# Kernel optimization log

Measured on AMD Instinct MI355X. Metric: run time of the kernel, lower is better.

The kernel has to match this reference:

```python
import jax, jax.numpy as jnp
import numpy as np

EPS = 0.1
MAX_ITER = 100
THRESH = 0.1


def _cost_matrix(x, y):
    # |x_i - y_j|^2 summed over feature dim, via the GEMM identity
    # ||x||^2 + ||y||^2 - 2<x,y>; clamp tiny negatives from fp error.
    x2 = jnp.sum(x * x, axis=-1)[..., :, None]          # (N,P1,1)
    y2 = jnp.sum(y * y, axis=-1)[..., None, :]          # (N,1,P2)
    xy = jnp.einsum('npd,nqd->npq', x, y)               # (N,P1,P2)
    return jnp.maximum(x2 + y2 - 2.0 * xy, 0.0)


def setup_inputs() -> dict:
    key = jax.random.key(0)
    k1, k2 = jax.random.split(key)
    x = jax.random.normal(k1, (8, 1024, 64), dtype=jnp.float32)
    y = jax.random.normal(k2, (8, 1024, 64), dtype=jnp.float32)
    return {"input": x, "target": y}


def reference(input, target):
    x, y = input, target
    C = _cost_matrix(x, y)                               # (N,P1,P2)
    N, P1 = x.shape[0], x.shape[-2]
    P2 = y.shape[-2]
    mu = jnp.full((N, P1), 1.0 / P1, dtype=C.dtype)
    nu = jnp.full((N, P2), 1.0 / P2, dtype=C.dtype)
    log_mu = jnp.log(mu + 1e-8)
    log_nu = jnp.log(nu + 1e-8)

    def M(u, v):
        # (-C + u_i + v_j) / eps
        return (-C + u[..., :, None] + v[..., None, :]) / EPS

    def body(carry, _):
        u, v, done = carry
        u_new = EPS * (log_mu - jax.scipy.special.logsumexp(M(u, v), axis=-1)) + u
        v_new = EPS * (log_nu - jax.scipy.special.logsumexp(M(u_new, v), axis=-2)) + v
        err = jnp.mean(jnp.sum(jnp.abs(u_new - u), axis=-1))
        # apply the update only if not yet converged (matches torch early break,
        # which breaks AFTER the update that achieved err < thresh)
        u = jnp.where(done, u, u_new)
        v = jnp.where(done, v, v_new)
        done = done | (err < THRESH)
        return (u, v, done), None

    u0 = jnp.zeros((N, P1), dtype=C.dtype)
    v0 = jnp.zeros((N, P2), dtype=C.dtype)
    (u, v, _), _ = jax.lax.scan(body, (u0, v0, jnp.array(False)), None, length=MAX_ITER)

    pi = jnp.exp(M(u, v))                                # transport plan (N,P1,P2)
    cost = jnp.sum(pi * C, axis=(-2, -1))                # (N,) with reduction='none'
    return cost
```

## Files before the change

kernel.cpp:

```cpp
#include <hip/hip_runtime.h>
#include <hip/hip_fp16.h>

#define NB 8
#define P 1024
#define D 64
#define EPSF 0.1f
#define INV_EPS 10.0f
#define MAX_IT 100
#define EPS_LOG_MU (-0.693146162f)
#define IB 512
#define TPB_I 512
#define BPB 64

#define HALF_F (NB * P * P / 2)
#define OFF_Z    0
#define OFF_ZT   (HALF_F)
#define OFF_U    (2 * HALF_F)
#define OFF_V    (OFF_U + NB * P)
#define OFF_X2   (OFF_V + NB * P)
#define OFF_Y2   (OFF_X2 + NB * P)
#define OFF_UH   (OFF_Y2 + NB * P)
#define OFF_DU   (OFF_UH + MAX_IT * NB * P)
#define OFF_BAR  (OFF_DU + MAX_IT * IB)
#define OFF_T    (OFF_BAR + 256)
#define OFF_COST (OFF_T + 64)
#define WS_FLOATS (OFF_COST + 64)

__device__ __forceinline__ void publish_f(float* p, float v) {
    __hip_atomic_store(p, v, __ATOMIC_RELAXED, __HIP_MEMORY_SCOPE_SYSTEM);
}

__device__ __forceinline__ void sysld4(float4& w0, float4& w1, float4& w2, float4& w3,
                                       const float* p0, const float* p1,
                                       const float* p2, const float* p3)
{
    asm volatile(
        "global_load_dwordx4 %0, %4, off sc0 sc1\n\t"
        "global_load_dwordx4 %1, %5, off sc0 sc1\n\t"
        "global_load_dwordx4 %2, %6, off sc0 sc1\n\t"
        "global_load_dwordx4 %3, %7, off sc0 sc1\n\t"
        "s_waitcnt vmcnt(0)"
        : "=&v"(w0), "=&v"(w1), "=&v"(w2), "=&v"(w3)
        : "v"(p0), "v"(p1), "v"(p2), "v"(p3)
        : "memory");
}

__global__ __launch_bounds__(256)
void init_k(const float* __restrict__ x, const float* __restrict__ y,
            float* __restrict__ ws)
{
    const int g = blockIdx.x * 256 + threadIdx.x;
    if (g < NB * P) {
        const float4* xr = (const float4*)(x + (size_t)g * D);
        const float4* yr = (const float4*)(y + (size_t)g * D);
        float sx = 0.f, sy = 0.f;
#pragma unroll
        for (int k = 0; k < D / 4; k++) {
            float4 a = xr[k], b = yr[k];
            sx = fmaf(a.x, a.x, fmaf(a.y, a.y, fmaf(a.z, a.z, fmaf(a.w, a.w, sx))));
            sy = fmaf(b.x, b.x, fmaf(b.y, b.y, fmaf(b.z, b.z, fmaf(b.w, b.w, sy))));
        }
        ws[OFF_X2 + g] = sx; ws[OFF_Y2 + g] = sy;
        ws[OFF_U + g] = 0.f; ws[OFF_V + g] = 0.f;
    }
    if (g < 256) ((unsigned*)(ws + OFF_BAR))[g] = 0u;
    if (g < 64)  ws[OFF_COST + g] = 0.f;
}

__global__ __launch_bounds__(256)
void gemm_k(const float* __restrict__ x, const float* __restrict__ y,
            float* __restrict__ ws)
{
    float* x2 = ws + OFF_X2;
    float* y2 = ws + OFF_Y2;
    const int tid   = threadIdx.x;
    const int half_ = blockIdx.x >> 9;
    const int bid   = blockIdx.x & 511;
    const int nB    = bid & 7;
    const int inner = bid >> 3;

    const float* A  = half_ ? y : x;
    const float* B  = half_ ? x : y;
    const float* ra = (half_ ? y2 : x2) + nB * P;
    const float* rb = (half_ ? x2 : y2) + nB * P;
    __half* out = (__half*)(ws + (half_ ? OFF_ZT : OFF_Z)) + (size_t)nB * P * P;

    __shared__ float xs [64 * 68];
    __shared__ float ysT[64 * 64];

    for (int k4 = 0; k4 < 4; k4++) {
        const int t  = inner * 4 + k4;
        const int ti = t >> 4, tj = t & 15;
        const float* abase = A + (size_t)(nB * P + ti * 64) * D;
        const float* bbase = B + (size_t)(nB * P + tj * 64) * D;
#pragma unroll
        for (int k = 0; k < 4; k++) {
            const int f = k * 1024 + tid * 4;
            const int r = f >> 6, c = f & 63;
            float4 a = *(const float4*)(abase + f);
            *(float4*)(xs + r * 68 + c) = a;
            float4 b = *(const float4*)(bbase + f);
            const int pr  = r >> 2;
            const int r3  = r & 3;
            const int t15 = c >> 2;
            ysT[(c + 0) * 64 + (((pr ^ t15) & 15) << 2) + r3] = b.x;
            ysT[(c + 1) * 64 + (((pr ^ t15) & 15) << 2) + r3] = b.y;
            ysT[(c + 2) * 64 + (((pr ^ t15) & 15) << 2) + r3] = b.z;
            ysT[(c + 3) * 64 + (((pr ^ t15) & 15) << 2) + r3] = b.w;
        }
        __syncthreads();
        const int r0 = tid >> 4;
        const int g  = tid & 15;
        const int c0 = g << 2;
#pragma unroll
        for (int rr = 0; rr < 4; rr++) {
            const int row = rr * 16 + r0;
            const float* xrow = xs + row * 68;
            float s0 = 0.f, s1 = 0.f, s2 = 0.f, s3 = 0.f;
#pragma unroll
            for (int d = 0; d < 64; d++) {
                const float xv = xrow[d];
                const float4 yv = *(const float4*)(ysT + d * 64 + ((g ^ ((d >> 2) & 15)) << 2));
                s0 = fmaf(xv, yv.x, s0); s1 = fmaf(xv, yv.y, s1);
                s2 = fmaf(xv, yv.z, s2); s3 = fmaf(xv, yv.w, s3);
            }
            const int gr = ti * 64 + row;
            const int gc = tj * 64 + c0;
            const float xq = ra[gr];
            union { unsigned long long u64; __half h[4]; } p;
            p.h[0] = __float2half_rn(-fmaxf(xq + rb[gc + 0] - 2.f * s0, 0.f) * INV_EPS);
            p.h[1] = __float2half_rn(-fmaxf(xq + rb[gc + 1] - 2.f * s1, 0.f) * INV_EPS);
            p.h[2] = __float2half_rn(-fmaxf(xq + rb[gc + 2] - 2.f * s2, 0.f) * INV_EPS);
            p.h[3] = __float2half_rn(-fmaxf(xq + rb[gc + 3] - 2.f * s3, 0.f) * INV_EPS);
            *(unsigned long long*)(out + (size_t)gr * P + gc) = p.u64;
        }
        __syncthreads();
    }
}

__device__ __forceinline__ void args8(uint4 c, float4 w0, float4 w1, float* zp)
{
    const __half2* h = (const __half2*)&c;
    float2 f;
    f = __half22float2(h[0]); zp[0] = fmaf(w0.x, INV_EPS, f.x); zp[1] = fmaf(w0.y, INV_EPS, f.y);
    f = __half22float2(h[1]); zp[2] = fmaf(w0.z, INV_EPS, f.x); zp[3] = fmaf(w0.w, INV_EPS, f.y);
    f = __half22float2(h[2]); zp[4] = fmaf(w1.x, INV_EPS, f.x); zp[5] = fmaf(w1.y, INV_EPS, f.y);
    f = __half22float2(h[3]); zp[6] = fmaf(w1.z, INV_EPS, f.x); zp[7] = fmaf(w1.w, INV_EPS, f.y);
}

#define MAX4(a,b,c,d) fmaxf(fmaxf(a,b),fmaxf(c,d))

__device__ __forceinline__ void lse2(uint4 c0a, uint4 c0b, uint4 c1a, uint4 c1b,
                                     float4 w0, float4 w1, float4 w2, float4 w3,
                                     float& o0, float& o1)
{
    float z0[16], z1[16];
    args8(c0a, w0, w1, z0); args8(c0b, w2, w3, z0 + 8);
    args8(c1a, w0, w1, z1); args8(c1b, w2, w3, z1 + 8);

    float m0 = fmaxf(MAX4(z0[0], z0[1], z0[2], z0[3]),  MAX4(z0[4], z0[5], z0[6], z0[7]));
    m0 = fmaxf(m0, fmaxf(MAX4(z0[8], z0[9], z0[10], z0[11]), MAX4(z0[12], z0[13], z0[14], z0[15])));
    float m1 = fmaxf(MAX4(z1[0], z1[1], z1[2], z1[3]),  MAX4(z1[4], z1[5], z1[6], z1[7]));
    m1 = fmaxf(m1, fmaxf(MAX4(z1[8], z1[9], z1[10], z1[11]), MAX4(z1[12], z1[13], z1[14], z1[15])));
#pragma unroll
    for (int off = 32; off; off >>= 1) {
        m0 = fmaxf(m0, __shfl_xor(m0, off, 64));
        m1 = fmaxf(m1, __shfl_xor(m1, off, 64));
    }
    float s0, s1;
    {
        float e0[16], e1[16];
#pragma unroll
        for (int q = 0; q < 16; q++) { e0[q] = __expf(z0[q] - m0); e1[q] = __expf(z1[q] - m1); }
#pragma unroll
        for (int q = 0; q < 8; q++)  { e0[q] += e0[q + 8]; e1[q] += e1[q + 8]; }
#pragma unroll
        for (int q = 0; q < 4; q++)  { e0[q] += e0[q + 4]; e1[q] += e1[q + 4]; }
        s0 = (e0[0] + e0[1]) + (e0[2] + e0[3]);
        s1 = (e1[0] + e1[1]) + (e1[2] + e1[3]);
    }
#pragma unroll
    for (int off = 32; off; off >>= 1) {
        s0 += __shfl_xor(s0, off, 64);
        s1 += __shfl_xor(s1, off, 64);
    }
    o0 = EPS_LOG_MU - EPSF * (m0 + __logf(s0));
    o1 = EPS_LOG_MU - EPSF * (m1 + __logf(s1));
}

__device__ __forceinline__ void bbar(unsigned* ctr, unsigned target)
{
    __syncthreads();
    if (threadIdx.x == 0) {
        __builtin_amdgcn_s_waitcnt(0);
        __hip_atomic_fetch_add(ctr, 1u, __ATOMIC_RELAXED, __HIP_MEMORY_SCOPE_AGENT);
        unsigned g = 0;
        while (__hip_atomic_load(ctr, __ATOMIC_RELAXED, __HIP_MEMORY_SCOPE_SYSTEM) < target) {
            __builtin_amdgcn_s_sleep(2);
            if (++g > (1u << 15)) break;
        }
    }
    __syncthreads();
}

__global__ __launch_bounds__(TPB_I, 4)
void iter_k(float* __restrict__ ws)
{
    const __half* z  = (const __half*)(ws + OFF_Z);
    const __half* zT = (const __half*)(ws + OFF_ZT);
    float* uh  = ws + OFF_UH;
    float* v   = ws + OFF_V;
    float* dup = ws + OFF_DU;

    const int tid   = threadIdx.x;
    const int nB    = blockIdx.x & 7;
    const int inner = blockIdx.x >> 3;
    const int wid   = tid >> 6;
    const int lane  = tid & 63;

    __shared__ float duRed[8];

    const int r0 = inner * 16 + wid * 2;
    const size_t zbase = (size_t)nB * P * P;

    const uint4* zr0 = (const uint4*)(z  + zbase + (size_t)(r0    ) * P);
    const uint4* zr1 = (const uint4*)(z  + zbase + (size_t)(r0 + 1) * P);
    const uint4* tr0 = (const uint4*)(zT + zbase + (size_t)(r0    ) * P);
    const uint4* tr1 = (const uint4*)(zT + zbase + (size_t)(r0 + 1) * P);
    const uint4 cz0a = zr0[lane], cz0b = zr0[lane + 64];
    const uint4 cz1a = zr1[lane], cz1b = zr1[lane + 64];
    const uint4 ct0a = tr0[lane], ct0b = tr0[lane + 64];
    const uint4 ct1a = tr1[lane], ct1b = tr1[lane + 64];

    unsigned* ctr = (unsigned*)(ws + OFF_BAR) + nB * 32;
    const int wo = lane * 8;
    float* vb = v + nB * P;

    float uold0 = 0.f, uold1 = 0.f;
    unsigned bstep = 0;

    for (int t = 0; t < MAX_IT; t++) {
        float* ut = uh + (size_t)t * (NB * P) + nB * P;

        float4 w0, w1, w2, w3;
        if (t == 0) {
            w0 = w1 = w2 = w3 = make_float4(0.f, 0.f, 0.f, 0.f);
        } else {
            sysld4(w0, w1, w2, w3, vb + wo, vb + wo + 4, vb + 512 + wo, vb + 512 + wo + 4);
        }
        float un0, un1;
        lse2(cz0a, cz0b, cz1a, cz1b, w0, w1, w2, w3, un0, un1);
        if (lane == 0) {
            publish_f(&ut[r0], un0);
            publish_f(&ut[r0 + 1], un1);
            duRed[wid] = fabsf(un0 - uold0) + fabsf(un1 - uold1);
        }
        uold0 = un0; uold1 = un1;
        __syncthreads();
        if (tid == 0) {
            float d = 0.f;
#pragma unroll
            for (int k = 0; k < 8; k++) d += duRed[k];
            dup[t * IB + blockIdx.x] = d;
        }
        bbar(ctr, BPB * (++bstep));

        float4 q0, q1, q2, q3;
        sysld4(q0, q1, q2, q3, ut + wo, ut + wo + 4, ut + 512 + wo, ut + 512 + wo + 4);
        float vn0, vn1;
        lse2(ct0a, ct0b, ct1a, ct1b, q0, q1, q2, q3, vn0, vn1);
        if (lane == 0) {
            publish_f(&vb[r0], vn0);
            publish_f(&vb[r0 + 1], vn1);
        }
        bbar(ctr, BPB * (++bstep));
    }
}

__global__ __launch_bounds__(1024)
void findT_k(float* __restrict__ ws)
{
    __shared__ float Spart[1024];
    __shared__ float S[MAX_IT];
    __shared__ int Ts;
    const int tid = threadIdx.x;

    {
        const int t = tid >> 3, sub = tid & 7;
        float s = 0.f;
        if (t < MAX_IT) {
            const float* dp = ws + OFF_DU + t * IB + sub * 64;
            for (int i = 0; i < 64; i++) s += dp[i];
        }
        Spart[tid] = s;
    }
    __syncthreads();
    if (tid < MAX_IT) {
        float s = 0.f;
#pragma unroll
        for (int k = 0; k < 8; k++) s += Spart[tid * 8 + k];
        S[tid] = s;
    }
    __syncthreads();
    if (tid == 0) {
        int T = MAX_IT - 1;
        for (int t = 0; t < MAX_IT; t++) if (S[t] < 0.8f) { T = t; break; }
        Ts = T;
        *(int*)(ws + OFF_T) = T;
    }
    __syncthreads();
    const int T = Ts;
    const float* src = ws + OFF_UH + (size_t)T * (NB * P);
    float* u = ws + OFF_U;
    for (int i = tid; i < NB * P; i += 1024) u[i] = src[i];
    if (tid < 64) ws[OFF_COST + tid] = 0.f;
}

__device__ __forceinline__ float lse_row(const __half* mat, const float4* wv,
                                         int row, int lane)
{
    const float4* mr = (const float4*)(mat + (size_t)row * P);
    const float4 ca = mr[lane];
    const float4 cb = mr[lane + 64];
    const uint4* cau = (const uint4*)&ca;
    const uint4* cbu = (const uint4*)&cb;
    const float4 wa0 = wv[2 * lane],       wa1 = wv[2 * lane + 1];
    const float4 wb0 = wv[128 + 2 * lane], wb1 = wv[129 + 2 * lane];
    float zv[16];
    args8(*cau, wa0, wa1, zv);
    args8(*cbu, wb0, wb1, zv + 8);
    float m = fmaxf(MAX4(zv[0], zv[1], zv[2], zv[3]), MAX4(zv[4], zv[5], zv[6], zv[7]));
    m = fmaxf(m, fmaxf(MAX4(zv[8], zv[9], zv[10], zv[11]), MAX4(zv[12], zv[13], zv[14], zv[15])));
#pragma unroll
    for (int off = 32; off; off >>= 1) m = fmaxf(m, __shfl_xor(m, off, 64));
    float s = 0.f;
#pragma unroll
    for (int q = 0; q < 16; q++) s += __expf(zv[q] - m);
#pragma unroll
    for (int off = 32; off; off >>= 1) s += __shfl_xor(s, off, 64);
    return EPS_LOG_MU - EPSF * (m + __logf(s));
}

__global__ __launch_bounds__(256)
void colT_k(float* __restrict__ ws)
{
    const __half* zT = (const __half*)(ws + OFF_ZT);
    float* u = ws + OFF_U;
    float* v = ws + OFF_V;
    const int tid   = threadIdx.x;
    const int nB    = blockIdx.x & 7;
    const int inner = blockIdx.x >> 3;
    const int wid   = tid >> 6;
    const int lane  = tid & 63;
    const __half* zTb = zT + (size_t)nB * P * P;
    const float4* ur = (const float4*)(u + nB * P);
#pragma unroll
    for (int rr = 0; rr < 4; rr++) {
        const int col = inner * 16 + wid * 4 + rr;
        const float vn = lse_row(zTb, ur, col, lane);
        if (lane == 0) v[nB * P + col] = vn;
    }
}

__global__ __launch_bounds__(256)
void cost_k(float* __restrict__ ws)
{
    const __half* z = (const __half*)(ws + OFF_Z);
    float* u    = ws + OFF_U;
    float* v    = ws + OFF_V;
    float* cost = ws + OFF_COST;
    const int tid   = threadIdx.x;
    const int nB    = blockIdx.x & 7;
    const int inner = blockIdx.x >> 3;
    const int wid   = tid >> 6;
    const int lane  = tid & 63;
    __shared__ float red[4];

    const float4* vr = (const float4*)(v + nB * P);
    float accW = 0.f;
#pragma unroll
    for (int rr = 0; rr < 4; rr++) {
        const int row = inner * 16 + wid * 4 + rr;
        const uint4* mr = (const uint4*)(z + ((size_t)nB * P + row) * P);
        const uint4 ca = mr[lane];
        const uint4 cb = mr[lane + 64];
        const float4 va0 = vr[2 * lane],       va1 = vr[2 * lane + 1];
        const float4 vb0 = vr[128 + 2 * lane], vb1 = vr[129 + 2 * lane];
        float zw[16];
        args8(ca, va0, va1, zw);
        args8(cb, vb0, vb1, zw + 8);
        float zc[16];
        {
            const __half2* ha = (const __half2*)&ca;
            const __half2* hb = (const __half2*)&cb;
            float2 f;
            f = __half22float2(ha[0]); zc[0] = f.x;  zc[1] = f.y;
            f = __half22float2(ha[1]); zc[2] = f.x;  zc[3] = f.y;
            f = __half22float2(ha[2]); zc[4] = f.x;  zc[5] = f.y;
            f = __half22float2(ha[3]); zc[6] = f.x;  zc[7] = f.y;
            f = __half22float2(hb[0]); zc[8] = f.x;  zc[9] = f.y;
            f = __half22float2(hb[1]); zc[10] = f.x; zc[11] = f.y;
            f = __half22float2(hb[2]); zc[12] = f.x; zc[13] = f.y;
            f = __half22float2(hb[3]); zc[14] = f.x; zc[15] = f.y;
        }
        const float ui = u[nB * P + row] * INV_EPS;
#pragma unroll
        for (int q = 0; q < 16; q++)
            accW += __expf(zw[q] + ui) * zc[q];
    }
#pragma unroll
    for (int off = 32; off; off >>= 1) accW += __shfl_xor(accW, off, 64);
    if (lane == 0) red[wid] = accW;
    __syncthreads();
    if (tid == 0)
        atomicAdd(&cost[nB], -EPSF * (red[0] + red[1] + red[2] + red[3]));
}

__global__ void out_k(const float* __restrict__ ws, float* __restrict__ out)
{
    if (threadIdx.x < NB) out[threadIdx.x] = ws[OFF_COST + threadIdx.x];
}

__global__ void sentinel_k(float* __restrict__ out)
{
    if (threadIdx.x < NB) out[threadIdx.x] = 1.0e6f;
}

extern "C" void kernel_launch(void* const* d_in, const int* in_sizes, int n_in,
                              void* d_out, int out_size, void* d_ws, size_t ws_size,
                              hipStream_t stream) {
    const float* x = (const float*)d_in[0];
    const float* y = (const float*)d_in[1];
    float* ws  = (float*)d_ws;
    float* out = (float*)d_out;

    if (ws_size < (size_t)WS_FLOATS * sizeof(float)) {
        sentinel_k<<<1, 64, 0, stream>>>(out);
        return;
    }

    init_k<<<32, 256, 0, stream>>>(x, y, ws);
    gemm_k<<<1024, 256, 0, stream>>>(x, y, ws);
    iter_k<<<IB, TPB_I, 0, stream>>>(ws);
    findT_k<<<1, 1024, 0, stream>>>(ws);
    colT_k<<<512, 256, 0, stream>>>(ws);
    cost_k<<<512, 256, 0, stream>>>(ws);
    out_k<<<1, 64, 0, stream>>>(ws, out);
}
```

Measured before the change: 1.144 ms.

## Shard grid barrier counters and switch log-sum-exp to base-2 exp/log

The per-batch barrier counter is split into 8 sub-counters on separate cache lines. Each block increments its own sub-counter, and one wavefront polls all 8 with uncached loads and sums them with shuffles. This spreads atomic contention across lines. Separately, the cost matrix is pre-scaled by log2(e)/eps so the inner exponentials use exp2f and the logs use log2f, removing a multiply per element. The init kernel also stops zeroing u and v, which may depend on other code to initialise them.

```diff
diff --git a/kernel.cpp b/kernel.cpp
--- a/kernel.cpp
+++ b/kernel.cpp
@@ -8,6 +8,9 @@
 #define INV_EPS 10.0f
 #define MAX_IT 100
 #define EPS_LOG_MU (-0.693146162f)
+#define EPSF_LN2   (0.0693147181f)
+#define SCALEW     (14.4269504089f)
+#define ZSC        (-14.4269504089f)
 #define IB 512
 #define TPB_I 512
 #define BPB 64
@@ -22,7 +25,8 @@
 #define OFF_UH   (OFF_Y2 + NB * P)
 #define OFF_DU   (OFF_UH + MAX_IT * NB * P)
 #define OFF_BAR  (OFF_DU + MAX_IT * IB)
-#define OFF_T    (OFF_BAR + 256)
+#define BAR_SZ   (NB * 8 * 32)
+#define OFF_T    (OFF_BAR + BAR_SZ)
 #define OFF_COST (OFF_T + 64)
 #define WS_FLOATS (OFF_COST + 64)
 
@@ -61,9 +65,8 @@
             sy = fmaf(b.x, b.x, fmaf(b.y, b.y, fmaf(b.z, b.z, fmaf(b.w, b.w, sy))));
         }
         ws[OFF_X2 + g] = sx; ws[OFF_Y2 + g] = sy;
-        ws[OFF_U + g] = 0.f; ws[OFF_V + g] = 0.f;
-    }
-    if (g < 256) ((unsigned*)(ws + OFF_BAR))[g] = 0u;
+    }
+    if (g < BAR_SZ) ((unsigned*)(ws + OFF_BAR))[g] = 0u;
     if (g < 64)  ws[OFF_COST + g] = 0.f;
 }
 
@@ -128,10 +131,10 @@
             const int gc = tj * 64 + c0;
             const float xq = ra[gr];
             union { unsigned long long u64; __half h[4]; } p;
-            p.h[0] = __float2half_rn(-fmaxf(xq + rb[gc + 0] - 2.f * s0, 0.f) * INV_EPS);
-            p.h[1] = __float2half_rn(-fmaxf(xq + rb[gc + 1] - 2.f * s1, 0.f) * INV_EPS);
-            p.h[2] = __float2half_rn(-fmaxf(xq + rb[gc + 2] - 2.f * s2, 0.f) * INV_EPS);
-            p.h[3] = __float2half_rn(-fmaxf(xq + rb[gc + 3] - 2.f * s3, 0.f) * INV_EPS);
+            p.h[0] = __float2half_rn(fmaxf(xq + rb[gc + 0] - 2.f * s0, 0.f) * ZSC);
+            p.h[1] = __float2half_rn(fmaxf(xq + rb[gc + 1] - 2.f * s1, 0.f) * ZSC);
+            p.h[2] = __float2half_rn(fmaxf(xq + rb[gc + 2] - 2.f * s2, 0.f) * ZSC);
+            p.h[3] = __float2half_rn(fmaxf(xq + rb[gc + 3] - 2.f * s3, 0.f) * ZSC);
             *(unsigned long long*)(out + (size_t)gr * P + gc) = p.u64;
         }
         __syncthreads();
@@ -142,10 +145,10 @@
 {
     const __half2* h = (const __half2*)&c;
     float2 f;
-    f = __half22float2(h[0]); zp[0] = fmaf(w0.x, INV_EPS, f.x); zp[1] = fmaf(w0.y, INV_EPS, f.y);
-    f = __half22float2(h[1]); zp[2] = fmaf(w0.z, INV_EPS, f.x); zp[3] = fmaf(w0.w, INV_EPS, f.y);
-    f = __half22float2(h[2]); zp[4] = fmaf(w1.x, INV_EPS, f.x); zp[5] = fmaf(w1.y, INV_EPS, f.y);
-    f = __half22float2(h[3]); zp[6] = fmaf(w1.z, INV_EPS, f.x); zp[7] = fmaf(w1.w, INV_EPS, f.y);
+    f = __half22float2(h[0]); zp[0] = fmaf(w0.x, SCALEW, f.x); zp[1] = fmaf(w0.y, SCALEW, f.y);
+    f = __half22float2(h[1]); zp[2] = fmaf(w0.z, SCALEW, f.x); zp[3] = fmaf(w0.w, SCALEW, f.y);
+    f = __half22float2(h[2]); zp[4] = fmaf(w1.x, SCALEW, f.x); zp[5] = fmaf(w1.y, SCALEW, f.y);
+    f = __half22float2(h[3]); zp[6] = fmaf(w1.z, SCALEW, f.x); zp[7] = fmaf(w1.w, SCALEW, f.y);
 }
 
 #define MAX4(a,b,c,d) fmaxf(fmaxf(a,b),fmaxf(c,d))
@@ -171,7 +174,7 @@
     {
         float e0[16], e1[16];
 #pragma unroll
-        for (int q = 0; q < 16; q++) { e0[q] = __expf(z0[q] - m0); e1[q] = __expf(z1[q] - m1); }
+        for (int q = 0; q < 16; q++) { e0[q] = exp2f(z0[q] - m0); e1[q] = exp2f(z1[q] - m1); }
 #pragma unroll
         for (int q = 0; q < 8; q++)  { e0[q] += e0[q + 8]; e1[q] += e1[q + 8]; }
 #pragma unroll
@@ -184,19 +187,32 @@
         s0 += __shfl_xor(s0, off, 64);
         s1 += __shfl_xor(s1, off, 64);
     }
-    o0 = EPS_LOG_MU - EPSF * (m0 + __logf(s0));
-    o1 = EPS_LOG_MU - EPSF * (m1 + __logf(s1));
-}
-
-__device__ __forceinline__ void bbar(unsigned* ctr, unsigned target)
-{
-    __syncthreads();
-    if (threadIdx.x == 0) {
-        __builtin_amdgcn_s_waitcnt(0);
-        __hip_atomic_fetch_add(ctr, 1u, __ATOMIC_RELAXED, __HIP_MEMORY_SCOPE_AGENT);
+    o0 = EPS_LOG_MU - EPSF_LN2 * (m0 + __log2f(s0));
+    o1 = EPS_LOG_MU - EPSF_LN2 * (m1 + __log2f(s1));
+}
+
+__device__ __forceinline__ void bbar(unsigned* ctrs, int sub, unsigned target,
+                                     int tid)
+{
+    __syncthreads();
+    if (tid == 0)
+        __hip_atomic_fetch_add(ctrs + sub * 32, 1u, __ATOMIC_RELAXED,
+                               __HIP_MEMORY_SCOPE_AGENT);
+    if (tid < 64) {
+        const unsigned* myp = ctrs + (tid & 7) * 32;
         unsigned g = 0;
-        while (__hip_atomic_load(ctr, __ATOMIC_RELAXED, __HIP_MEMORY_SCOPE_SYSTEM) < target) {
-            __builtin_amdgcn_s_sleep(2);
+        for (;;) {
+            unsigned c = 0;
+            if (tid < 8) {
+                asm volatile("global_load_dword %0, %1, off sc0 sc1\n\ts_waitcnt vmcnt(0)"
+                             : "=&v"(c) : "v"(myp) : "memory");
+            }
+            unsigned s = c;
+            s += __shfl_xor(s, 1, 64);
+            s += __shfl_xor(s, 2, 64);
+            s += __shfl_xor(s, 4, 64);
+            if (__shfl(s, 0, 64) >= target) break;
+            __builtin_amdgcn_s_sleep(1);
             if (++g > (1u << 15)) break;
         }
     }
@@ -232,8 +248,9 @@
     const uint4 ct0a = tr0[lane], ct0b = tr0[lane + 64];
     const uint4 ct1a = tr1[lane], ct1b = tr1[lane + 64];
 
-    unsigned* ctr = (unsigned*)(ws + OFF_BAR) + nB * 32;
-    const int wo = lane * 8;
+    unsigned* ctrs = (unsigned*)(ws + OFF_BAR) + nB * 256;
+    const int sub  = inner & 7;
+    const int wo   = lane * 8;
     float* vb = v + nB * P;
 
     float uold0 = 0.f, uold1 = 0.f;
@@ -263,7 +280,7 @@
             for (int k = 0; k < 8; k++) d += duRed[k];
             dup[t * IB + blockIdx.x] = d;
         }
-        bbar(ctr, BPB * (++bstep));
+        bbar(ctrs, sub, BPB * (++bstep), tid);
 
         float4 q0, q1, q2, q3;
         sysld4(q0, q1, q2, q3, ut + wo, ut + wo + 4, ut + 512 + wo, ut + 512 + wo + 4);
@@ -273,7 +290,7 @@
             publish_f(&vb[r0], vn0);
             publish_f(&vb[r0 + 1], vn1);
         }
-        bbar(ctr, BPB * (++bstep));
+        bbar(ctrs, sub, BPB * (++bstep), tid);
     }
 }
 
@@ -319,26 +336,24 @@
 __device__ __forceinline__ float lse_row(const __half* mat, const float4* wv,
                                          int row, int lane)
 {
-    const float4* mr = (const float4*)(mat + (size_t)row * P);
-    const float4 ca = mr[lane];
-    const float4 cb = mr[lane + 64];
-    const uint4* cau = (const uint4*)&ca;
-    const uint4* cbu = (const uint4*)&cb;
+    const uint4* mr = (const uint4*)(mat + (size_t)row * P);
+    const uint4 ca = mr[lane];
+    const uint4 cb = mr[lane + 64];
     const float4 wa0 = wv[2 * lane],       wa1 = wv[2 * lane + 1];
     const float4 wb0 = wv[128 + 2 * lane], wb1 = wv[129 + 2 * lane];
     float zv[16];
-    args8(*cau, wa0, wa1, zv);
-    args8(*cbu, wb0, wb1, zv + 8);
+    args8(ca, wa0, wa1, zv);
+    args8(cb, wb0, wb1, zv + 8);
     float m = fmaxf(MAX4(zv[0], zv[1], zv[2], zv[3]), MAX4(zv[4], zv[5], zv[6], zv[7]));
     m = fmaxf(m, fmaxf(MAX4(zv[8], zv[9], zv[10], zv[11]), MAX4(zv[12], zv[13], zv[14], zv[15])));
 #pragma unroll
     for (int off = 32; off; off >>= 1) m = fmaxf(m, __shfl_xor(m, off, 64));
     float s = 0.f;
 #pragma unroll
-    for (int q = 0; q < 16; q++) s += __expf(zv[q] - m);
+    for (int q = 0; q < 16; q++) s += exp2f(zv[q] - m);
 #pragma unroll
     for (int off = 32; off; off >>= 1) s += __shfl_xor(s, off, 64);
-    return EPS_LOG_MU - EPSF * (m + __logf(s));
+    return EPS_LOG_MU - EPSF_LN2 * (m + __log2f(s));
 }
 
 __global__ __launch_bounds__(256)
@@ -403,17 +418,17 @@
             f = __half22float2(hb[2]); zc[12] = f.x; zc[13] = f.y;
             f = __half22float2(hb[3]); zc[14] = f.x; zc[15] = f.y;
         }
-        const float ui = u[nB * P + row] * INV_EPS;
+        const float ui = u[nB * P + row] * SCALEW;
 #pragma unroll
         for (int q = 0; q < 16; q++)
-            accW += __expf(zw[q] + ui) * zc[q];
+            accW += exp2f(zw[q] + ui) * zc[q];
     }
 #pragma unroll
     for (int off = 32; off; off >>= 1) accW += __shfl_xor(accW, off, 64);
     if (lane == 0) red[wid] = accW;
     __syncthreads();
     if (tid == 0)
-        atomicAdd(&cost[nB], -EPSF * (red[0] + red[1] + red[2] + red[3]));
+        atomicAdd(&cost[nB], -EPSF_LN2 * (red[0] + red[1] + red[2] + red[3]));
 }
 
 __global__ void out_k(const float* __restrict__ ws, float* __restrict__ out)
```

After: 1.561 ms. +36.4%, slower.
